# Kernel optimization log

Measured on AMD Instinct MI355X. Metric: run time of the kernel, lower is better.

The kernel has to match this reference:

```python
import jax, jax.numpy as jnp
import numpy as np
import math

B, S, H, NH, NKV = 4, 2048, 2048, 16, 8
HD = H // NH           # 128
N_REP = NH // NKV      # 2


def rotate_half(t):
    t1, t2 = jnp.split(t, 2, axis=-1)
    return jnp.concatenate([-t2, t1], axis=-1)


def setup_inputs() -> dict:
    key = jax.random.key(0)
    ks = jax.random.split(key, 6)
    x = jax.random.normal(ks[0], (B, S, H), dtype=jnp.float32)
    # realistic RoPE tables [max_pos, head_dim]
    inv_freq = 1.0 / (10000.0 ** (np.arange(0, HD, 2, dtype=np.float32) / HD))
    t = np.arange(S, dtype=np.float32)
    freqs = np.outer(t, inv_freq)                 # [S, HD/2]
    emb = np.concatenate([freqs, freqs], axis=-1)  # [S, HD]
    cos = jnp.asarray(np.cos(emb), dtype=jnp.float32)
    sin = jnp.asarray(np.sin(emb), dtype=jnp.float32)
    sc = 0.02
    Wq = jax.random.normal(ks[1], (H, NH * HD), dtype=jnp.float32) * sc
    Wk = jax.random.normal(ks[2], (H, NKV * HD), dtype=jnp.float32) * sc
    Wv = jax.random.normal(ks[3], (H, NKV * HD), dtype=jnp.float32) * sc
    Wo = jax.random.normal(ks[4], (NH * HD, H), dtype=jnp.float32) * sc
    return {"x": x, "cos": cos, "sin": sin, "Wq": Wq, "Wk": Wk, "Wv": Wv, "Wo": Wo}


def reference(x, cos, sin, Wq, Wk, Wv, Wo):
    bsz, seq_len, _ = x.shape
    xq = (x @ Wq).reshape(bsz, seq_len, NH, HD)
    xk = (x @ Wk).reshape(bsz, seq_len, NKV, HD)
    xv = (x @ Wv).reshape(bsz, seq_len, NKV, HD)

    # RoPE (past_len = 0, no cache)
    c = cos[:seq_len][None, :, None, :]   # [1,S,1,HD]
    s = sin[:seq_len][None, :, None, :]
    xq = xq * c + rotate_half(xq) * s
    xk = xk * c + rotate_half(xk) * s

    # repeat_kv (GQA): [B,S,NKV,HD] -> [B,S,NH,HD]
    xk = jnp.repeat(xk, N_REP, axis=2)
    xv = jnp.repeat(xv, N_REP, axis=2)

    q = xq.transpose(0, 2, 1, 3)  # [B,NH,S,HD]
    k = xk.transpose(0, 2, 1, 3)
    v = xv.transpose(0, 2, 1, 3)

    scores = jnp.einsum('bhqd,bhkd->bhqk', q, k) / math.sqrt(HD)
    causal = jnp.triu(jnp.full((seq_len, seq_len), -jnp.inf, dtype=scores.dtype), k=1)
    scores = scores + causal[None, None]
    probs = jax.nn.softmax(scores.astype(jnp.float32), axis=-1).astype(q.dtype)
    out = jnp.einsum('bhqk,bhkd->bhqd', probs, v)
    out = out.transpose(0, 2, 1, 3).reshape(bsz, seq_len, NH * HD)
    return out @ Wo
```

## Files before the change

### kernel.cpp

```cpp
#include <hip/hip_runtime.h>
#include <stdint.h>

using bf16   = __bf16;
using bf16x4 = __attribute__((ext_vector_type(4))) __bf16;
using bf16x8 = __attribute__((ext_vector_type(8))) __bf16;
using f32x4  = __attribute__((ext_vector_type(4))) float;

#define DEV_INLINE __device__ __forceinline__

DEV_INLINE void gload16(const void* g, const void* l) {
  __builtin_amdgcn_global_load_lds(
      (const __attribute__((address_space(1))) unsigned int*)(uintptr_t)g,
      (__attribute__((address_space(3))) unsigned int*)(unsigned int)(uintptr_t)l,
      16, 0, 0);
}

DEV_INLINE f32x4 mfma16(bf16x8 a, bf16x8 b, f32x4 c) {
  return __builtin_amdgcn_mfma_f32_16x16x32_bf16(a, b, c, 0, 0, 0);
}

#define WAIT_LGKM0() do { \
  asm volatile("s_waitcnt lgkmcnt(0)" ::: "memory"); \
  __builtin_amdgcn_sched_barrier(0); } while (0)

__global__ void cast_f32_bf16(const float4* __restrict__ in, bf16* __restrict__ out, int n4) {
  int i = blockIdx.x * 256 + threadIdx.x;
  if (i >= n4) return;
  float4 v = in[i];
  bf16x4 o = { (bf16)v.x, (bf16)v.y, (bf16)v.z, (bf16)v.w };
  *(bf16x4*)(out + (size_t)i * 4) = o;
}

__global__ void transpose_cast(const float* __restrict__ in, bf16* __restrict__ out,
                               int rows, int cols) {
  __shared__ float tile[32][33];
  int c0 = blockIdx.x * 32, r0 = blockIdx.y * 32;
  int t = threadIdx.x, tc = t & 31, tr = t >> 5;
  for (int i = 0; i < 4; ++i)
    tile[tr + i*8][tc] = in[(size_t)(r0 + tr + i*8) * cols + (c0 + tc)];
  __syncthreads();
  for (int i = 0; i < 4; ++i)
    out[(size_t)(c0 + tr + i*8) * rows + (r0 + tc)] = (bf16)tile[tc][tr + i*8];
}


DEV_INLINE void stage_half(const bf16* __restrict__ src, int K, int k0, bf16* slot,
                           int w, int lr, int lc) {
#pragma unroll
  for (int i = 0; i < 2; ++i)
    gload16(src + (size_t)(w*16 + lr) * K + (k0 + i*32 + lc*8), slot + (w*2 + i) * 512);
}

DEV_INLINE void load_afr(bf16x8 (&af)[4][2], const bf16* slot, int wr2, int l) {
#pragma unroll
  for (int mi = 0; mi < 4; ++mi)
#pragma unroll
    for (int ks = 0; ks < 2; ++ks)
      af[mi][ks] = *(const bf16x8*)(slot + ((wr2*4 + mi)*2 + ks) * 512 + l*8);
}

template<bool PERM>
DEV_INLINE void load_bfr(bf16x8 (&bfr)[2][2], const bf16* slot, int wc2, int l) {
#pragma unroll
  for (int ni = 0; ni < 2; ++ni)
#pragma unroll
    for (int ks = 0; ks < 2; ++ks) {
      int mt = PERM ? (ni*4 + wc2) : (wc2*2 + ni);
      bfr[ni][ks] = *(const bf16x8*)(slot + (mt*2 + ks) * 512 + l*8);
    }
}

DEV_INLINE void mfma_quad(f32x4 (&aq)[4][2], const bf16x8 (&af)[4][2],
                          const bf16x8 (&bfr)[2][2]) {
#pragma unroll
  for (int mi = 0; mi < 4; ++mi)
#pragma unroll
    for (int ni = 0; ni < 2; ++ni)
#pragma unroll
      for (int ks = 0; ks < 2; ++ks)
        aq[mi][ni] = mfma16(af[mi][ks], bfr[ni][ks], aq[mi][ni]);
}

template<bool PERM, int K, int NK>
DEV_INLINE void gemm256_core(const bf16* __restrict__ A, const bf16* __restrict__ Bt,
                             int bm0, int bn0, bf16* sA, bf16* sB,
                             int w, int l, int lr, int lc, int wr2, int wc2,
                             f32x4 (&acc)[2][2][4][2]) {
  const bf16* Ar0 = A  + (size_t)bm0 * K;
  const bf16* Ar1 = Ar0 + (size_t)128 * K;
  const bf16* Br0 = Bt + (size_t)bn0 * K;
  const bf16* Br1 = Br0 + (size_t)128 * K;
  stage_half(Ar0, K, 0,  sA + 0*8192, w, lr, lc);
  stage_half(Br1, K, 0,  sB + 1*8192, w, lr, lc);
  stage_half(Ar1, K, 0,  sA + 1*8192, w, lr, lc);
  stage_half(Br0, K, 0,  sB + 0*8192, w, lr, lc);
  stage_half(Ar0, K, 64, sA + 2*8192, w, lr, lc);
  stage_half(Br1, K, 64, sB + 3*8192, w, lr, lc);
  __syncthreads();

  for (int kt = 0; kt < NK; ++kt) {
    const int k1 = (kt + 1 < NK ? kt + 1 : 0) * 64;
    const int k2 = (kt + 2 < NK ? kt + 2 : 0) * 64;
    bf16* A0s = sA + ((2*kt    ) & 3) * 8192;
    bf16* A1s = sA + ((2*kt + 1) & 3) * 8192;
    bf16* B0s = sB + ((2*kt    ) & 3) * 8192;
    bf16* B1s = sB + ((2*kt + 1) & 3) * 8192;
    bf16x8 af[4][2], bfr[2][2];

    load_afr(af, A0s, wr2, l);
    load_bfr<PERM>(bfr, B0s, wc2, l);
    stage_half(Ar1, K, k1, sA + ((2*kt + 3) & 3) * 8192, w, lr, lc);
    __builtin_amdgcn_s_barrier();
    WAIT_LGKM0();
    __builtin_amdgcn_s_setprio(1);
    mfma_quad(acc[0][0], af, bfr);
    __builtin_amdgcn_s_setprio(0);
    __builtin_amdgcn_s_barrier();

    load_bfr<PERM>(bfr, B1s, wc2, l);
    stage_half(Br0, K, k1, sB + ((2*kt + 2) & 3) * 8192, w, lr, lc);
    __builtin_amdgcn_s_barrier();
    WAIT_LGKM0();
    __builtin_amdgcn_s_setprio(1);
    mfma_quad(acc[0][1], af, bfr);
    __builtin_amdgcn_s_setprio(0);
    __builtin_amdgcn_s_barrier();

    load_afr(af, A1s, wr2, l);
    stage_half(Ar0, K, k2, sA + ((2*kt + 4) & 3) * 8192, w, lr, lc);
    __builtin_amdgcn_s_barrier();
    WAIT_LGKM0();
    __builtin_amdgcn_s_setprio(1);
    mfma_quad(acc[1][1], af, bfr);
    __builtin_amdgcn_s_setprio(0);
    __builtin_amdgcn_s_barrier();

    load_bfr<PERM>(bfr, B0s, wc2, l);
    stage_half(Br1, K, k2, sB + ((2*kt + 5) & 3) * 8192, w, lr, lc);
    __builtin_amdgcn_s_barrier();
    WAIT_LGKM0();
    __builtin_amdgcn_s_setprio(1);
    mfma_quad(acc[1][0], af, bfr);
    __builtin_amdgcn_s_setprio(0);
    asm volatile("s_waitcnt vmcnt(4)" ::: "memory");
    __builtin_amdgcn_sched_barrier(0);
    __builtin_amdgcn_s_barrier();
  }
  asm volatile("s_waitcnt vmcnt(0)" ::: "memory");
}

__global__ __launch_bounds__(512, 2)
void gemm256_rope(const bf16* __restrict__ A, const bf16* __restrict__ Bt,
                  const float* __restrict__ cs, const float* __restrict__ sn,
                  bf16* __restrict__ Qr, bf16* __restrict__ Kr,
                  bf16* __restrict__ Vbuf) {
  __shared__ bf16 sA[4 * 8192];
  __shared__ bf16 sB[4 * 8192];
  int id = blockIdx.x;
  int swz = (id & 7) * 64 + (id >> 3);
  int tm = swz >> 4, tn = swz & 15;
  int bm0 = tm * 256, bn0 = tn * 256;
  int tid = threadIdx.x, w = tid >> 6, l = tid & 63, lr = l & 15, lc = l >> 4;
  int wr2 = w >> 2, wc2 = w & 3;
  f32x4 acc[2][2][4][2] = {};
  gemm256_core<true, 2048, 32>(A, Bt, bm0, bn0, sA, sB, w, l, lr, lc, wr2, wc2, acc);

  int bb = bm0 >> 11, s0 = bm0 & 2047;
  int dlo = wc2 * 16 + lr;
#pragma unroll
  for (int nh = 0; nh < 2; ++nh) {
    int h128 = tn * 2 + nh;
    if (h128 < 24) {
      const float scale = (h128 < 16) ? 0.08838834764831845f * 1.4426950408889634f : 1.0f;
      bf16* dstB = (h128 < 16)
          ? Qr + (size_t)(bb * 16 + h128) * 2048 * 128
          : Kr + (size_t)(bb * 8 + (h128 - 16)) * 2048 * 128;
#pragma unroll
      for (int mh = 0; mh < 2; ++mh)
#pragma unroll
        for (int mi = 0; mi < 4; ++mi)
#pragma unroll
          for (int r = 0; r < 4; ++r) {
            int sl = s0 + mh*128 + wr2*64 + mi*16 + lc*4 + r;
            float c  = cs[sl * 128 + dlo];
            float sv = sn[sl * 128 + dlo];
            float lo = acc[mh][nh][mi][0][r], hi = acc[mh][nh][mi][1][r];
            bf16* dst = dstB + (size_t)sl * 128 + dlo;
            dst[0]  = (bf16)((lo * c - hi * sv) * scale);
            dst[64] = (bf16)((hi * c + lo * sv) * scale);
          }
    } else {
      int kvh = h128 - 24;
#pragma unroll
      for (int mh = 0; mh < 2; ++mh)
#pragma unroll
        for (int mi = 0; mi < 4; ++mi)
#pragma unroll
          for (int r = 0; r < 4; ++r) {
            int sl = s0 + mh*128 + wr2*64 + mi*16 + lc*4 + r;
            bf16* dst = Vbuf + ((size_t)(bb * 2048) + sl) * 1024 + kvh * 128 + dlo;
            dst[0]  = (bf16)acc[mh][nh][mi][0][r];
            dst[64] = (bf16)acc[mh][nh][mi][1][r];
          }
    }
  }
}

__global__ __launch_bounds__(512, 2)
void gemm256_out(const bf16* __restrict__ A, const bf16* __restrict__ Bt,
                 float* __restrict__ C) {
  __shared__ bf16 sA[4 * 8192];
  __shared__ bf16 sB[4 * 8192];
  int id = blockIdx.x;
  int swz = (id & 7) * 32 + (id >> 3);
  int tm = swz >> 3, tn = swz & 7;
  int bm0 = tm * 256, bn0 = tn * 256;
  int tid = threadIdx.x, w = tid >> 6, l = tid & 63, lr = l & 15, lc = l >> 4;
  int wr2 = w >> 2, wc2 = w & 3;
  f32x4 acc[2][2][4][2] = {};
  gemm256_core<false, 2048, 32>(A, Bt, bm0, bn0, sA, sB, w, l, lr, lc, wr2, wc2, acc);
#pragma unroll
  for (int mh = 0; mh < 2; ++mh)
#pragma unroll
    for (int nh = 0; nh < 2; ++nh)
#pragma unroll
      for (int mi = 0; mi < 4; ++mi)
#pragma unroll
        for (int ni = 0; ni < 2; ++ni)
#pragma unroll
          for (int r = 0; r < 4; ++r) {
            int row = bm0 + mh*128 + wr2*64 + mi*16 + lc*4 + r;
            int col = bn0 + nh*128 + wc2*32 + ni*16 + lr;
            C[(size_t)row * 2048 + col] = acc[mh][nh][mi][ni][r];
          }
}

__global__ void v_transpose(const bf16* __restrict__ Vbuf, bf16* __restrict__ Vt) {
  __shared__ bf16 tile[32][33];
  int s0 = blockIdx.x * 32, d0 = blockIdx.y * 32, bh = blockIdx.z;
  int b = bh >> 3, h = bh & 7;
  int t = threadIdx.x, tc = t & 31, tr = t >> 5;
  for (int i = 0; i < 4; ++i)
    tile[tr + i*8][tc] =
        Vbuf[((size_t)(b*2048) + s0 + tr + i*8) * 1024 + h*128 + d0 + tc];
  __syncthreads();
  for (int i = 0; i < 4; ++i)
    Vt[((size_t)bh * 128 + d0 + tr + i*8) * 2048 + s0 + tc] = tile[tc][tr + i*8];
}

__global__ __launch_bounds__(512, 2)
void attn_kernel(const bf16* __restrict__ Q, const bf16* __restrict__ Kg,
                 const bf16* __restrict__ Vt, bf16* __restrict__ Og) {
  __shared__ bf16 sK[32 * 512];
  __shared__ bf16 sV[32 * 512];
  int x = blockIdx.x, y = blockIdx.y;
  int qi = (x + (y >> 1)) & 15;
  int bkv = y;
  int b = bkv >> 3, kvh = bkv & 7;
  int tid = threadIdx.x, w = tid >> 6, l = tid & 63, lr = l & 15, lc = l >> 4;
  const bf16* Qb0 = Q + ((size_t)(b*16 + kvh*2) * 2048 + qi*128) * 128;
  const bf16* Qb1 = Qb0 + (size_t)2048 * 128;
  const bf16* Kb  = Kg + (size_t)bkv * 2048 * 128;
  const bf16* Vb  = Vt + (size_t)bkv * 128 * 2048;
  bf16x8 qf0[4], qf1[4];
  for (int ks = 0; ks < 4; ++ks) {
    size_t off = (size_t)(w*16 + lr) * 128 + ks*32 + lc*8;
    qf0[ks] = *(const bf16x8*)(Qb0 + off);
    qf1[ks] = *(const bf16x8*)(Qb1 + off);
  }
  f32x4 o0[8] = {}, o1[8] = {};
  float l0[4] = {0.f,0.f,0.f,0.f}, l1[4] = {0.f,0.f,0.f,0.f};
  int qrow = qi*128 + w*16 + lc*4;
  bf16* sPw = sK + w * 2048;
  int tmax = qi + 1;
  for (int t = 0; t < tmax; ++t) {
    __syncthreads();
    for (int i = 0; i < 4; ++i) {
      int id = w*4 + i;
      int nt = id >> 2, ks = id & 3;
      gload16(Kb + (size_t)(t*128 + nt*16 + lr) * 128 + ks*32 + lc*8, sK + id*512);
      gload16(Vb + (size_t)(nt*16 + lr) * 2048 + t*128 + ks*32 + lc*8, sV + id*512);
    }
    __syncthreads();
    f32x4 s0[8] = {}, s1[8] = {};
    for (int nt = 0; nt < 8; ++nt)
      for (int ks = 0; ks < 4; ++ks) {
        bf16x8 kf = *(const bf16x8*)(sK + (nt*4 + ks)*512 + l*8);
        s0[nt] = mfma16(qf0[ks], kf, s0[nt]);
        s1[nt] = mfma16(qf1[ks], kf, s1[nt]);
      }
    if (t == tmax - 1) {
      for (int nt = 0; nt < 8; ++nt) {
        int col = t*128 + nt*16 + lr;
        for (int r = 0; r < 4; ++r)
          if (col > qrow + r) { s0[nt][r] = -1e30f; s1[nt][r] = -1e30f; }
      }
    }
    __syncthreads();
    bf16x8 pf0[4], pf1[4];
    for (int nt = 0; nt < 8; ++nt) {
      int hi6 = (nt >> 2) * 1024;
      int blk = (nt*2 + (lr >> 3)) & 7;
      int off = lr & 7;
      for (int r = 0; r < 4; ++r) {
        int q = lc*4 + r;
        float p = __builtin_amdgcn_exp2f(s0[nt][r]);
        l0[r] += p;
        sPw[hi6 + q*64 + ((blk ^ (q & 7)) * 8) + off] = (bf16)p;
      }
    }
    WAIT_LGKM0();
    for (int ks = 0; ks < 4; ++ks)
      pf0[ks] = *(const bf16x8*)(sPw + (ks >> 1)*1024 + lr*64 +
                                 ((((ks & 1)*4 + lc) ^ (lr & 7)) * 8));
    WAIT_LGKM0();
    for (int nt = 0; nt < 8; ++nt) {
      int hi6 = (nt >> 2) * 1024;
      int blk = (nt*2 + (lr >> 3)) & 7;
      int off = lr & 7;
      for (int r = 0; r < 4; ++r) {
        int q = lc*4 + r;
        float p = __builtin_amdgcn_exp2f(s1[nt][r]);
        l1[r] += p;
        sPw[hi6 + q*64 + ((blk ^ (q & 7)) * 8) + off] = (bf16)p;
      }
    }
    WAIT_LGKM0();
    for (int ks = 0; ks < 4; ++ks)
      pf1[ks] = *(const bf16x8*)(sPw + (ks >> 1)*1024 + lr*64 +
                                 ((((ks & 1)*4 + lc) ^ (lr & 7)) * 8));
    for (int nt = 0; nt < 8; ++nt)
      for (int ks = 0; ks < 4; ++ks) {
        bf16x8 vf = *(const bf16x8*)(sV + (nt*4 + ks)*512 + l*8);
        o0[nt] = mfma16(pf0[ks], vf, o0[nt]);
        o1[nt] = mfma16(pf1[ks], vf, o1[nt]);
      }
  }
  for (int msk = 1; msk < 16; msk <<= 1)
    for (int r = 0; r < 4; ++r) {
      l0[r] += __shfl_xor(l0[r], msk, 64);
      l1[r] += __shfl_xor(l1[r], msk, 64);
    }
  for (int r = 0; r < 4; ++r) {
    float inv0 = 1.f / l0[r];
    float inv1 = 1.f / l1[r];
    size_t row = (size_t)(b*2048) + qi*128 + w*16 + lc*4 + r;
    size_t base0 = row * 2048 + (kvh*2) * 128;
    for (int nt = 0; nt < 8; ++nt) {
      Og[base0 + nt*16 + lr]       = (bf16)(o0[nt][r] * inv0);
      Og[base0 + 128 + nt*16 + lr] = (bf16)(o1[nt][r] * inv1);
    }
  }
}

extern "C" void kernel_launch(void* const* d_in, const int* in_sizes, int n_in,
                              void* d_out, int out_size, void* d_ws, size_t ws_size,
                              hipStream_t stream) {
  (void)in_sizes; (void)n_in; (void)out_size; (void)ws_size;
  const float* x  = (const float*)d_in[0];
  const float* cs = (const float*)d_in[1];
  const float* sn = (const float*)d_in[2];
  const float* Wq = (const float*)d_in[3];
  const float* Wk = (const float*)d_in[4];
  const float* Wv = (const float*)d_in[5];
  const float* Wo = (const float*)d_in[6];
  float* out = (float*)d_out;

  char* p = (char*)d_ws;
  bf16* xb    = (bf16*)p;  p += (size_t)8192*2048*2;
  bf16* Wt    = (bf16*)p;  p += (size_t)4096*2048*2;
  bf16* Wot   = (bf16*)p;  p += (size_t)2048*2048*2;
  bf16* Qr    = (bf16*)p;  p += (size_t)64*2048*128*2;
  bf16* Kr    = (bf16*)p;  p += (size_t)32*2048*128*2;
  bf16* Vbuf  = (bf16*)p;  p += (size_t)8192*1024*2;
  bf16* Vtb   = (bf16*)p;  p += (size_t)32*2048*128*2;
  bf16* attnb = (bf16*)p;  p += (size_t)8192*2048*2;

  cast_f32_bf16<<<4194304/256, 256, 0, stream>>>((const float4*)x, xb, 4194304);
  transpose_cast<<<dim3(64,64), 256, 0, stream>>>(Wq, Wt, 2048, 2048);
  transpose_cast<<<dim3(32,64), 256, 0, stream>>>(Wk, Wt + (size_t)2048*2048, 2048, 1024);
  transpose_cast<<<dim3(32,64), 256, 0, stream>>>(Wv, Wt + (size_t)3072*2048, 2048, 1024);
  transpose_cast<<<dim3(64,64), 256, 0, stream>>>(Wo, Wot, 2048, 2048);
  gemm256_rope<<<dim3(512), 512, 0, stream>>>(xb, Wt, cs, sn, Qr, Kr, Vbuf);
  v_transpose<<<dim3(64,4,32), 256, 0, stream>>>(Vbuf, Vtb);
  attn_kernel<<<dim3(16,32), 512, 0, stream>>>(Qr, Kr, Vtb, attnb);
  gemm256_out<<<dim3(256), 512, 0, stream>>>(attnb, Wot, out);
}
```

Baseline: 565.1 us.

## Double-buffer K/V tiles in LDS to prefetch next tile during compute

Doubles the K and V shared-memory buffers and issues global-to-LDS loads for tile t+1 before computing on tile t, waiting with a partial vmcnt so the current tile's loads complete first. This aims to overlap global memory latency with the QK and PV MFMA work instead of stalling on each tile load. It doubles LDS use to 128KB per block, which may cut occupancy below the two blocks per CU requested by launch bounds. It also relies on hand-placed raw barriers and waitcnt counts for correctness.

```diff
diff --git a/kernel.cpp b/kernel.cpp
--- a/kernel.cpp
+++ b/kernel.cpp
@@ -21,6 +21,11 @@
 
 #define WAIT_LGKM0() do { \
   asm volatile("s_waitcnt lgkmcnt(0)" ::: "memory"); \
+  __builtin_amdgcn_sched_barrier(0); } while (0)
+
+#define RAW_BARRIER() do { \
+  __builtin_amdgcn_sched_barrier(0); \
+  __builtin_amdgcn_s_barrier(); \
   __builtin_amdgcn_sched_barrier(0); } while (0)
 
 __global__ void cast_f32_bf16(const float4* __restrict__ in, bf16* __restrict__ out, int n4) {
@@ -251,8 +256,8 @@
 __global__ __launch_bounds__(512, 2)
 void attn_kernel(const bf16* __restrict__ Q, const bf16* __restrict__ Kg,
                  const bf16* __restrict__ Vt, bf16* __restrict__ Og) {
-  __shared__ bf16 sK[32 * 512];
-  __shared__ bf16 sV[32 * 512];
+  __shared__ bf16 sK[2][32 * 512];
+  __shared__ bf16 sV[2][32 * 512];
   int x = blockIdx.x, y = blockIdx.y;
   int qi = (x + (y >> 1)) & 15;
   int bkv = y;
@@ -271,21 +276,39 @@
   f32x4 o0[8] = {}, o1[8] = {};
   float l0[4] = {0.f,0.f,0.f,0.f}, l1[4] = {0.f,0.f,0.f,0.f};
   int qrow = qi*128 + w*16 + lc*4;
-  bf16* sPw = sK + w * 2048;
   int tmax = qi + 1;
+
+#pragma unroll
+  for (int i = 0; i < 4; ++i) {
+    int id = w*4 + i, nt = id >> 2, ks = id & 3;
+    gload16(Kb + (size_t)(nt*16 + lr) * 128 + ks*32 + lc*8, sK[0] + id*512);
+    gload16(Vb + (size_t)(nt*16 + lr) * 2048 + ks*32 + lc*8, sV[0] + id*512);
+  }
+
   for (int t = 0; t < tmax; ++t) {
-    __syncthreads();
-    for (int i = 0; i < 4; ++i) {
-      int id = w*4 + i;
-      int nt = id >> 2, ks = id & 3;
-      gload16(Kb + (size_t)(t*128 + nt*16 + lr) * 128 + ks*32 + lc*8, sK + id*512);
-      gload16(Vb + (size_t)(nt*16 + lr) * 2048 + t*128 + ks*32 + lc*8, sV + id*512);
-    }
-    __syncthreads();
+    int cur = t & 1;
+    bf16* sKc = sK[cur];
+    bf16* sVc = sV[cur];
+    RAW_BARRIER();
+    if (t + 1 < tmax) {
+#pragma unroll
+      for (int i = 0; i < 4; ++i) {
+        int id = w*4 + i, nt = id >> 2, ks = id & 3;
+        gload16(Kb + (size_t)((t+1)*128 + nt*16 + lr) * 128 + ks*32 + lc*8,
+                sK[cur ^ 1] + id*512);
+        gload16(Vb + (size_t)(nt*16 + lr) * 2048 + (t+1)*128 + ks*32 + lc*8,
+                sV[cur ^ 1] + id*512);
+      }
+      asm volatile("s_waitcnt vmcnt(8)" ::: "memory");
+    } else {
+      asm volatile("s_waitcnt vmcnt(0)" ::: "memory");
+    }
+    __builtin_amdgcn_sched_barrier(0);
+    RAW_BARRIER();
     f32x4 s0[8] = {}, s1[8] = {};
     for (int nt = 0; nt < 8; ++nt)
       for (int ks = 0; ks < 4; ++ks) {
-        bf16x8 kf = *(const bf16x8*)(sK + (nt*4 + ks)*512 + l*8);
+        bf16x8 kf = *(const bf16x8*)(sKc + (nt*4 + ks)*512 + l*8);
         s0[nt] = mfma16(qf0[ks], kf, s0[nt]);
         s1[nt] = mfma16(qf1[ks], kf, s1[nt]);
       }
@@ -296,7 +319,9 @@
           if (col > qrow + r) { s0[nt][r] = -1e30f; s1[nt][r] = -1e30f; }
       }
     }
-    __syncthreads();
+    WAIT_LGKM0();
+    RAW_BARRIER();
+    bf16* sPw = sKc + w * 2048;
     bf16x8 pf0[4], pf1[4];
     for (int nt = 0; nt < 8; ++nt) {
       int hi6 = (nt >> 2) * 1024;
@@ -331,10 +356,11 @@
                                  ((((ks & 1)*4 + lc) ^ (lr & 7)) * 8));
     for (int nt = 0; nt < 8; ++nt)
       for (int ks = 0; ks < 4; ++ks) {
-        bf16x8 vf = *(const bf16x8*)(sV + (nt*4 + ks)*512 + l*8);
+        bf16x8 vf = *(const bf16x8*)(sVc + (nt*4 + ks)*512 + l*8);
         o0[nt] = mfma16(pf0[ks], vf, o0[nt]);
         o1[nt] = mfma16(pf1[ks], vf, o1[nt]);
       }
+    WAIT_LGKM0();
   }
   for (int msk = 1; msk < 16; msk <<= 1)
     for (int r = 0; r < 4; ++r) {
```

New measurement: 545.8 us. 3.4% less time.
